# Kernel tuning notes

Hardware: AMD Instinct MI355X
Metric: run time of the kernel (lower is better)

The kernel has to match this reference:

```python
import jax, jax.numpy as jnp
import numpy as np

NUM_HEADS = 4
NUM_GROUPS = 8
EPS = 1e-5


def setup_inputs() -> dict:
    key = jax.random.key(0)
    ks = jax.random.split(key, 4)
    B, C, H, W = 16, 512, 64, 64
    x = jax.random.normal(ks[0], (B, C, H, W), dtype=jnp.float32)
    norm_g = jnp.ones((C,), dtype=jnp.float32)
    norm_b = jnp.zeros((C,), dtype=jnp.float32)
    qkv_w = jax.random.normal(ks[1], (3 * C, C), dtype=jnp.float32) * (1.0 / np.sqrt(C))
    qkv_b = jnp.zeros((3 * C,), dtype=jnp.float32)
    proj_w = jax.random.normal(ks[2], (C, C), dtype=jnp.float32) * (1.0 / np.sqrt(C))
    proj_b = jnp.zeros((C,), dtype=jnp.float32)
    return {"x": x, "norm_g": norm_g, "norm_b": norm_b,
            "qkv_w": qkv_w, "qkv_b": qkv_b, "proj_w": proj_w, "proj_b": proj_b}


def _group_norm(x, g, b):
    B, C, H, W = x.shape
    xg = x.reshape(B, NUM_GROUPS, C // NUM_GROUPS, H, W)
    mean = xg.mean(axis=(2, 3, 4), keepdims=True)
    var = xg.var(axis=(2, 3, 4), keepdims=True)
    xn = ((xg - mean) * jax.lax.rsqrt(var + EPS)).reshape(B, C, H, W)
    return xn * g[None, :, None, None] + b[None, :, None, None]


def reference(x, norm_g, norm_b, qkv_w, qkv_b, proj_w, proj_b):
    B, C, H, W = x.shape
    d = C // NUM_HEADS
    scale = d ** (-0.5)
    xn = _group_norm(x, norm_g, norm_b)
    # 1x1 conv == channel GEMM
    qkv = jnp.einsum('oc,bchw->bohw', qkv_w, xn) + qkv_b[None, :, None, None]
    qkv = qkv.reshape(B, NUM_HEADS, 3 * d, H * W)
    q, k, v = qkv[:, :, :d], qkv[:, :, d:2 * d], qkv[:, :, 2 * d:]
    # Faithful to the original (degenerate) einsum: q's last axis is summed out
    attn = jnp.einsum('bnhq,bnhk->bnhk', q, k) * scale
    attn = jax.nn.softmax(attn, axis=-1)
    out = jnp.einsum('bnhk,bnhv->bnhv', attn, v)
    out = out.reshape(B, C, H, W)
    out = jnp.einsum('oc,bchw->bohw', proj_w, out) + proj_b[None, :, None, None]
    return out + x
```

## Files before the change

kernel.cpp:

```cpp
#include <hip/hip_runtime.h>

#define CC 512
#define SS 4096
#define GELEMS 262144

typedef __attribute__((ext_vector_type(8))) __bf16 bf16x8;
typedef __attribute__((ext_vector_type(4))) float f32x4;
typedef __attribute__((ext_vector_type(4))) unsigned short us4;
typedef __attribute__((ext_vector_type(8))) unsigned short us8;

__device__ __forceinline__ unsigned short f2bf(float f) {
  unsigned int u = __float_as_uint(f);
  u += 0x7fffu + ((u >> 16) & 1u);
  return (unsigned short)(u >> 16);
}
__device__ __forceinline__ int qrow(int cv) { return ((cv >> 7) * 384) + 256 + (cv & 127); }

__device__ __forceinline__ void gl_lds16(const void* g, void* l) {
  __builtin_amdgcn_global_load_lds((const __attribute__((address_space(1))) unsigned int*)g,
                                   (__attribute__((address_space(3))) unsigned int*)l, 16, 0, 0);
}

__global__ __launch_bounds__(256) void k_front(const float* __restrict__ x,
    const float* __restrict__ pw, const float* __restrict__ qw,
    unsigned short* __restrict__ xbft, float* __restrict__ part, float* __restrict__ mw) {
  __shared__ float red[8];
  __shared__ __align__(16) unsigned short G[8 * 512];
  __shared__ __align__(16) unsigned short Asb[64 * 32];
  __shared__ __align__(16) unsigned short Bsb[64 * 32];
  int t = threadIdx.x;
  if (blockIdx.x < 8192) {
    int bid = blockIdx.x;
    int b = bid >> 9, rem = bid & 511, ct = rem >> 6, st = rem & 63;
    int c0 = ct * 64, s0 = st * 64;
    int w = t >> 6, l = t & 63;
    int ch4 = l >> 4, s4 = l & 15;
    int cbase = w * 16 + ch4;
    float4 vv[4];
#pragma unroll
    for (int i = 0; i < 4; ++i) {
      int c = cbase + i * 4;
      vv[i] = *(const float4*)&x[((size_t)(b * 512 + c0 + c)) * SS + s0 + s4 * 4];
    }
    float sm = 0.f, sq = 0.f;
#pragma unroll
    for (int i = 0; i < 4; ++i) {
      sm += vv[i].x + vv[i].y + vv[i].z + vv[i].w;
      sq += vv[i].x * vv[i].x + vv[i].y * vv[i].y + vv[i].z * vv[i].z + vv[i].w * vv[i].w;
    }
#pragma unroll
    for (int off = 32; off; off >>= 1) { sm += __shfl_down(sm, off); sq += __shfl_down(sq, off); }
    if (l == 0) { red[w] = sm; red[4 + w] = sq; }
#pragma unroll
    for (int i = 0; i < 4; ++i) {
      int c = cbase + i * 4, g = c >> 3, chl = c & 7;
      float e[4] = {vv[i].x, vv[i].y, vv[i].z, vv[i].w};
#pragma unroll
      for (int j = 0; j < 4; ++j) {
        int s = s4 * 4 + j, slot = s ^ (s >> 3);
        G[g * 512 + slot * 8 + chl] = f2bf(e[j]);
      }
    }
    __syncthreads();
    if (t == 0) {
      int pidx = (b * 8 + ct) * 64 + st;
      part[pidx * 2] = red[0] + red[1] + red[2] + red[3];
      part[pidx * 2 + 1] = red[4] + red[5] + red[6] + red[7];
    }
    unsigned short* tb = xbft + ((size_t)(b * 64 + st)) * 32768;
    int slot = l ^ (l >> 3);
    int jj = l >> 4, frr = l & 15;
#pragma unroll
    for (int h = 0; h < 2; ++h) {
      int g = w * 2 + h;
      us8 v = *(const us8*)&G[g * 512 + slot * 8];
      int k8g = ct * 8 + g;
      int kc = k8g >> 4, s8l = (k8g >> 2) & 3, fql = k8g & 3;
      *(us8*)&tb[kc * 8192 + (s8l * 4 + jj) * 512 + (fql * 16 + frr) * 8] = v;
    }
  } else {
    int bb = blockIdx.x - 8192;
    int bm = (bb >> 3) * 64;
    int bn = (bb & 7) * 64;
    int w = t >> 6, l = t & 63;
    int wm = (w >> 1) * 32, wn = (w & 1) * 32;
    int fr = l & 15, fk = (l >> 4) * 8;
    f32x4 acc[2][2] = {};
    for (int k0 = 0; k0 < 512; k0 += 32) {
#pragma unroll
      for (int i = 0; i < 2; ++i) {
        int e = i * 256 + t;
        int row = e >> 3, f4 = e & 7;
        float4 v = *(const float4*)&pw[(size_t)(bm + row) * 512 + k0 + f4 * 4];
        us4 pk; pk[0] = f2bf(v.x); pk[1] = f2bf(v.y); pk[2] = f2bf(v.z); pk[3] = f2bf(v.w);
        *(us4*)&Asb[row * 32 + f4 * 4] = pk;
      }
#pragma unroll
      for (int i = 0; i < 2; ++i) {
        int e = i * 256 + t;
        int row = e >> 4, f4 = e & 15;
        float4 v = *(const float4*)&qw[(size_t)qrow(k0 + row) * 512 + bn + f4 * 4];
        Bsb[(f4 * 4 + 0) * 32 + row] = f2bf(v.x);
        Bsb[(f4 * 4 + 1) * 32 + row] = f2bf(v.y);
        Bsb[(f4 * 4 + 2) * 32 + row] = f2bf(v.z);
        Bsb[(f4 * 4 + 3) * 32 + row] = f2bf(v.w);
      }
      __syncthreads();
      bf16x8 a[2], bfr[2];
#pragma unroll
      for (int i = 0; i < 2; ++i) a[i] = *(const bf16x8*)&Asb[(wm + i * 16 + fr) * 32 + fk];
#pragma unroll
      for (int j = 0; j < 2; ++j) bfr[j] = *(const bf16x8*)&Bsb[(wn + j * 16 + fr) * 32 + fk];
#pragma unroll
      for (int i = 0; i < 2; ++i)
#pragma unroll
        for (int j = 0; j < 2; ++j)
          acc[i][j] = __builtin_amdgcn_mfma_f32_16x16x32_bf16(a[i], bfr[j], acc[i][j], 0, 0, 0);
      __syncthreads();
    }
#pragma unroll
    for (int i = 0; i < 2; ++i)
#pragma unroll
      for (int j = 0; j < 2; ++j)
#pragma unroll
        for (int r = 0; r < 4; ++r) {
          int row = bm + wm + i * 16 + (l >> 4) * 4 + r;
          int col = bn + wn + j * 16 + (l & 15);
          mw[(size_t)row * 512 + col] = acc[i][j][r];
        }
  }
}

__global__ __launch_bounds__(256) void k_prep(const float* __restrict__ part,
    const float* __restrict__ ng, const float* __restrict__ nb,
    const float* __restrict__ mw, const float* __restrict__ pw,
    const float* __restrict__ qb, const float* __restrict__ pb,
    unsigned short* __restrict__ mwa, float* __restrict__ bias2) {
  int t = threadIdx.x;
  __shared__ float S1[512], S2[512];
  __shared__ float ms[8], rs[8];
  int b = (blockIdx.x < 2048) ? (blockIdx.x >> 7) : ((blockIdx.x - 2048) >> 3);
  {
    int g = t >> 5, i = t & 31;
    const float* p = part + (size_t)(b * 8 + g) * 128;
    float S = p[i * 2] + p[(i + 32) * 2];
    float Q = p[i * 2 + 1] + p[(i + 32) * 2 + 1];
#pragma unroll
    for (int off = 16; off; off >>= 1) { S += __shfl_down(S, off, 32); Q += __shfl_down(Q, off, 32); }
    if (i == 0) {
      float mean = S * (1.f / 262144.f);
      float var = Q * (1.f / 262144.f) - mean * mean;
      ms[g] = mean; rs[g] = rsqrtf(var + 1e-5f);
    }
  }
  __syncthreads();
  if (blockIdx.x < 2048) {
    int r4 = (blockIdx.x & 127) * 4;
#pragma unroll
    for (int q = 0; q < 2; ++q) { int c = t + q * 256; S1[c] = rs[c >> 6] * ng[c]; }
    __syncthreads();
    int c2 = r4 + (t >> 6), c = (t & 63) * 8;
    const float4* mr = (const float4*)&mw[(size_t)c2 * 512 + c];
    float4 m0 = mr[0], m1 = mr[1];
    const float4* ar = (const float4*)&S1[c];
    float4 a0 = ar[0], a1 = ar[1];
    float v[8] = {m0.x*a0.x, m0.y*a0.y, m0.z*a0.z, m0.w*a0.w,
                  m1.x*a1.x, m1.y*a1.y, m1.z*a1.z, m1.w*a1.w};
    if (c2 >= c && c2 < c + 8) v[c2 - c] += 1.0f;
    us8 o;
#pragma unroll
    for (int j = 0; j < 8; ++j) o[j] = f2bf(v[j]);
    int wblk = c2 >> 6, i2 = (c2 >> 4) & 3, fr = c2 & 15;
    int step = c >> 5, fq = (c >> 3) & 3;
    size_t addr = ((((size_t)(b * 8 + wblk) * 4 + i2) * 16 + step) * 64 + (fq * 16 + fr)) * 8;
    *(us8*)&mwa[addr] = o;
  } else {
    int c2b = ((blockIdx.x - 2048) & 7) * 64;
    int w = t >> 6, l = t & 63;
#pragma unroll
    for (int q = 0; q < 2; ++q) {
      int c = t + q * 256;
      float A = rs[c >> 6] * ng[c];
      S1[c] = nb[c] - ms[c >> 6] * A;
      S2[c] = qb[qrow(c)];
    }
    __syncthreads();
    for (int it = 0; it < 16; ++it) {
      int c2 = c2b + w * 16 + it;
      const float4* pwr = (const float4*)&pw[(size_t)c2 * 512];
      const float4* mwr = (const float4*)&mw[(size_t)c2 * 512];
      float4 p0 = pwr[l * 2], p1 = pwr[l * 2 + 1];
      float4 m0 = mwr[l * 2], m1 = mwr[l * 2 + 1];
      const float4* qs = (const float4*)&S2[l * 8];
      const float4* bs = (const float4*)&S1[l * 8];
      float4 q0 = qs[0], q1 = qs[1], b0 = bs[0], b1 = bs[1];
      float acc = p0.x * q0.x + p0.y * q0.y + p0.z * q0.z + p0.w * q0.w
                + p1.x * q1.x + p1.y * q1.y + p1.z * q1.z + p1.w * q1.w
                + m0.x * b0.x + m0.y * b0.y + m0.z * b0.z + m0.w * b0.w
                + m1.x * b1.x + m1.y * b1.y + m1.z * b1.z + m1.w * b1.w;
#pragma unroll
      for (int off = 32; off; off >>= 1) acc += __shfl_down(acc, off);
      if (l == 0) bias2[b * 512 + c2] = acc + pb[c2];
    }
  }
}

__global__ __launch_bounds__(512, 4) void k_fused5(const unsigned short* __restrict__ mwa,
    const unsigned short* __restrict__ xbft, const float* __restrict__ bias2,
    float* __restrict__ out) {
  __shared__ __align__(16) unsigned short Bs[2][8192];
  int bid0 = blockIdx.x;
  int bid = 1023 - ((bid0 & 7) * 128 + (bid0 >> 3));
  int b = bid >> 6, st = bid & 63;
  int s0 = st * 64;
  int t = threadIdx.x, w = t >> 6, l = t & 63;
  int m0 = w * 64;
  int fr = l & 15, fq = l >> 4;
  const unsigned short* tile = xbft + ((size_t)(b * 64 + st)) * 32768;
  const unsigned short* Ag = mwa + ((size_t)(b * 8 + w)) * 32768;

  auto stage = [&](int buf, int kc) {
    const unsigned short* src = tile + kc * 8192 + w * 1024 + l * 8;
    gl_lds16(src, &Bs[buf][w * 1024]);
    gl_lds16(src + 512, &Bs[buf][w * 1024 + 512]);
  };

  stage(0, 0);
  bf16x8 fa[2][4];
#pragma unroll
  for (int i = 0; i < 4; ++i)
    fa[0][i] = *(const bf16x8*)&Ag[(i * 16 + 0) * 512 + l * 8];
  __syncthreads();

  f32x4 acc[4][4] = {};
#pragma unroll
  for (int kc = 0; kc < 4; ++kc) {
    if (kc < 3) stage((kc + 1) & 1, kc + 1);
#pragma unroll
    for (int s8 = 0; s8 < 4; ++s8) {
      const int step = kc * 4 + s8;
      const int cur = step & 1;
      if (step < 15) {
#pragma unroll
        for (int i = 0; i < 4; ++i)
          fa[cur ^ 1][i] = *(const bf16x8*)&Ag[(i * 16 + step + 1) * 512 + l * 8];
      }
      bf16x8 fb[4];
#pragma unroll
      for (int j = 0; j < 4; ++j)
        fb[j] = *(const bf16x8*)&Bs[kc & 1][(s8 * 4 + j) * 512 + l * 8];
#pragma unroll
      for (int i = 0; i < 4; ++i)
#pragma unroll
        for (int j = 0; j < 4; ++j)
          acc[i][j] = __builtin_amdgcn_mfma_f32_16x16x32_bf16(fa[cur][i], fb[j], acc[i][j], 0, 0, 0);
    }
    if (kc < 3) __syncthreads();
  }

  float4 bi[4];
#pragma unroll
  for (int i = 0; i < 4; ++i)
    bi[i] = *(const float4*)&bias2[b * 512 + m0 + i * 16 + fq * 4];
  __syncthreads();
  float* Ls = (float*)Bs;
  float* ob = out + (size_t)b * 512 * SS + s0;
#pragma unroll
  for (int i = 0; i < 4; ++i) {
    float bir[4] = {bi[i].x, bi[i].y, bi[i].z, bi[i].w};
#pragma unroll
    for (int j = 0; j < 4; ++j)
#pragma unroll
      for (int r = 0; r < 4; ++r)
        Ls[w * 1024 + (fq * 4 + r) * 64 + (((j ^ fq) & 3) * 16 + fr)] = acc[i][j][r] + bir[r];
    asm volatile("s_waitcnt lgkmcnt(0)" ::: "memory");
    __builtin_amdgcn_sched_barrier(0);
#pragma unroll
    for (int q = 0; q < 4; ++q) {
      int row16 = q * 4 + (l >> 4);
      int colR = (l & 15) * 4;
      f32x4 v = *(const f32x4*)&Ls[w * 1024 + row16 * 64 + (colR ^ (q * 16))];
      __builtin_nontemporal_store(v, (f32x4*)&ob[(size_t)(m0 + i * 16 + row16) * SS + colR]);
    }
    asm volatile("s_waitcnt lgkmcnt(0)" ::: "memory");
  }
}

__global__ __launch_bounds__(256) void k_stats(const float* __restrict__ x, float* __restrict__ part) {
  int bid = blockIdx.x;
  int bg = bid >> 3, sp = bid & 7;
  const float4* p = (const float4*)(x + (size_t)bg * GELEMS + (size_t)sp * 32768);
  int t = threadIdx.x;
  float s = 0.f, ss = 0.f;
#pragma unroll
  for (int i = 0; i < 32; ++i) {
    float4 v = p[i * 256 + t];
    s += v.x + v.y + v.z + v.w;
    ss += v.x * v.x + v.y * v.y + v.z * v.z + v.w * v.w;
  }
#pragma unroll
  for (int off = 32; off; off >>= 1) { s += __shfl_down(s, off); ss += __shfl_down(ss, off); }
  __shared__ float red[8];
  int wid = t >> 6;
  if ((t & 63) == 0) { red[wid * 2] = s; red[wid * 2 + 1] = ss; }
  __syncthreads();
  if (t == 0) {
    part[bid * 2] = red[0] + red[2] + red[4] + red[6];
    part[bid * 2 + 1] = red[1] + red[3] + red[5] + red[7];
  }
}

__global__ __launch_bounds__(256) void k_mw(const float* __restrict__ pw, const float* __restrict__ qw,
                                            float* __restrict__ mw, unsigned short* __restrict__ mwbf) {
  __shared__ __align__(16) unsigned short Asb[64 * 32];
  __shared__ __align__(16) unsigned short Bsb[64 * 32];
  int t = threadIdx.x;
  int bm = (blockIdx.x >> 3) * 64;
  int bn = (blockIdx.x & 7) * 64;
  int w = t >> 6, l = t & 63;
  int wm = (w >> 1) * 32, wn = (w & 1) * 32;
  int fr = l & 15, fk = (l >> 4) * 8;
  f32x4 acc[2][2] = {};
  for (int k0 = 0; k0 < 512; k0 += 32) {
#pragma unroll
    for (int i = 0; i < 2; ++i) {
      int e = i * 256 + t;
      int row = e >> 3, f4 = e & 7;
      float4 v = *(const float4*)&pw[(size_t)(bm + row) * 512 + k0 + f4 * 4];
      us4 pk; pk[0] = f2bf(v.x); pk[1] = f2bf(v.y); pk[2] = f2bf(v.z); pk[3] = f2bf(v.w);
      *(us4*)&Asb[row * 32 + f4 * 4] = pk;
    }
#pragma unroll
    for (int i = 0; i < 2; ++i) {
      int e = i * 256 + t;
      int row = e >> 4, f4 = e & 15;
      float4 v = *(const float4*)&qw[(size_t)qrow(k0 + row) * 512 + bn + f4 * 4];
      Bsb[(f4 * 4 + 0) * 32 + row] = f2bf(v.x);
      Bsb[(f4 * 4 + 1) * 32 + row] = f2bf(v.y);
      Bsb[(f4 * 4 + 2) * 32 + row] = f2bf(v.z);
      Bsb[(f4 * 4 + 3) * 32 + row] = f2bf(v.w);
    }
    __syncthreads();
    bf16x8 a[2], bfr[2];
#pragma unroll
    for (int i = 0; i < 2; ++i) a[i] = *(const bf16x8*)&Asb[(wm + i * 16 + fr) * 32 + fk];
#pragma unroll
    for (int j = 0; j < 2; ++j) bfr[j] = *(const bf16x8*)&Bsb[(wn + j * 16 + fr) * 32 + fk];
#pragma unroll
    for (int i = 0; i < 2; ++i)
#pragma unroll
      for (int j = 0; j < 2; ++j)
        acc[i][j] = __builtin_amdgcn_mfma_f32_16x16x32_bf16(a[i], bfr[j], acc[i][j], 0, 0, 0);
    __syncthreads();
  }
#pragma unroll
  for (int i = 0; i < 2; ++i)
#pragma unroll
    for (int j = 0; j < 2; ++j)
#pragma unroll
      for (int r = 0; r < 4; ++r) {
        int row = bm + wm + i * 16 + (l >> 4) * 4 + r;
        int col = bn + wn + j * 16 + (l & 15);
        float v = acc[i][j][r];
        mw[(size_t)row * 512 + col] = v;
        mwbf[(size_t)row * 512 + col] = f2bf(v);
      }
}

__global__ __launch_bounds__(256) void k_fin(const float* __restrict__ part,
    const float* __restrict__ ng, const float* __restrict__ nb,
    float* __restrict__ afac, float* __restrict__ bcv, int np) {
  int b = blockIdx.x, t = threadIdx.x;
  __shared__ float mean_s[8], rstd_s[8];
  int g = t >> 5, i = t & 31;
  float S = 0.f, Q = 0.f;
  for (int k = i; k < np; k += 32) {
    S += part[((b * 8 + g) * np + k) * 2];
    Q += part[((b * 8 + g) * np + k) * 2 + 1];
  }
#pragma unroll
  for (int off = 16; off; off >>= 1) { S += __shfl_down(S, off, 32); Q += __shfl_down(Q, off, 32); }
  if (i == 0) {
    float mean = S * (1.f / 262144.f);
    float var = Q * (1.f / 262144.f) - mean * mean;
    mean_s[g] = mean;
    rstd_s[g] = rsqrtf(var + 1e-5f);
  }
  __syncthreads();
#pragma unroll
  for (int q = 0; q < 2; ++q) {
    int c = t + q * 256;
    int gg = c >> 6;
    float A = rstd_s[gg] * ng[c];
    afac[b * 512 + c] = A;
    bcv[b * 512 + c] = nb[c] - mean_s[gg] * A;
  }
}

__global__ __launch_bounds__(256) void k_bias2(const float* __restrict__ mw,
    const float* __restrict__ bcv, const float* __restrict__ pw,
    const float* __restrict__ qb, const float* __restrict__ pb, float* __restrict__ bias2) {
  int b = blockIdx.x >> 3, c2b = (blockIdx.x & 7) * 64;
  int t = threadIdx.x, w = t >> 6, l = t & 63;
  __shared__ float Bcs[512], Qbs[512];
  for (int i = t; i < 512; i += 256) { Bcs[i] = bcv[b * 512 + i]; Qbs[i] = qb[qrow(i)]; }
  __syncthreads();
  for (int it = 0; it < 16; ++it) {
    int c2 = c2b + w * 16 + it;
    const float4* pwr = (const float4*)&pw[(size_t)c2 * 512];
    const float4* mwr = (const float4*)&mw[(size_t)c2 * 512];
    float4 p0 = pwr[l * 2], p1 = pwr[l * 2 + 1];
    float4 m0 = mwr[l * 2], m1 = mwr[l * 2 + 1];
    const float4* qs = (const float4*)&Qbs[l * 8];
    const float4* bs = (const float4*)&Bcs[l * 8];
    float4 q0 = qs[0], q1 = qs[1], b0 = bs[0], b1 = bs[1];
    float acc = p0.x * q0.x + p0.y * q0.y + p0.z * q0.z + p0.w * q0.w
              + p1.x * q1.x + p1.y * q1.y + p1.z * q1.z + p1.w * q1.w
              + m0.x * b0.x + m0.y * b0.y + m0.z * b0.z + m0.w * b0.w
              + m1.x * b1.x + m1.y * b1.y + m1.z * b1.z + m1.w * b1.w;
#pragma unroll
    for (int off = 32; off; off >>= 1) acc += __shfl_down(acc, off);
    if (l == 0) bias2[b * 512 + c2] = acc + pb[c2];
  }
}

__global__ __launch_bounds__(256) void k_gemm_fb(const unsigned short* __restrict__ mwbf,
    const float* __restrict__ x, const float* __restrict__ afac,
    const float* __restrict__ bias2, float* __restrict__ out) {
  __shared__ __align__(16) unsigned short Ab[128 * 32];
  __shared__ __align__(16) unsigned short Bb[128 * 32];
  __shared__ float Afs[512];
  int bid0 = blockIdx.x;
  int bid = (bid0 & 7) * 256 + (bid0 >> 3);
  int b = bid >> 7, rem = bid & 127, nt = rem >> 2, mt = rem & 3;
  int m0 = mt * 128, s0 = nt * 128;
  int t = threadIdx.x, w = t >> 6, l = t & 63;
  int wm = (w >> 1) * 64, wn = (w & 1) * 64;
  const unsigned short* Ag = mwbf + (size_t)m0 * CC;
  int lr = l >> 2, lk = (l & 3) * 8;
  int fr = l & 15, fk = (l >> 4) * 8;
  for (int i = t; i < 512; i += 256) Afs[i] = afac[b * CC + i];
  __syncthreads();
  f32x4 acc[4][4] = {};
  for (int k0 = 0; k0 < CC; k0 += 32) {
#pragma unroll
    for (int q = 0; q < 2; ++q) {
      int row = w * 32 + q * 16;
      gl_lds16(Ag + (size_t)(row + lr) * CC + k0 + lk, &Ab[row * 32]);
    }
#pragma unroll
    for (int i2 = 0; i2 < 4; ++i2) {
      int e = i2 * 256 + t;
      int row = e >> 5, f4 = e & 31;
      float4 v = *(const float4*)&x[((size_t)(b * CC + k0 + row)) * SS + s0 + f4 * 4];
      float a = Afs[k0 + row];
      Bb[(f4 * 4 + 0) * 32 + row] = f2bf(v.x * a);
      Bb[(f4 * 4 + 1) * 32 + row] = f2bf(v.y * a);
      Bb[(f4 * 4 + 2) * 32 + row] = f2bf(v.z * a);
      Bb[(f4 * 4 + 3) * 32 + row] = f2bf(v.w * a);
    }
    __syncthreads();
    bf16x8 af[4], bfr[4];
#pragma unroll
    for (int i = 0; i < 4; ++i) af[i] = *(const bf16x8*)&Ab[(wm + i * 16 + fr) * 32 + fk];
#pragma unroll
    for (int j = 0; j < 4; ++j) bfr[j] = *(const bf16x8*)&Bb[(wn + j * 16 + fr) * 32 + fk];
#pragma unroll
    for (int i = 0; i < 4; ++i)
#pragma unroll
      for (int j = 0; j < 4; ++j)
        acc[i][j] = __builtin_amdgcn_mfma_f32_16x16x32_bf16(af[i], bfr[j], acc[i][j], 0, 0, 0);
    __syncthreads();
  }
  int c2b = m0 + wm, sb = s0 + wn;
  float bi[4][4];
#pragma unroll
  for (int i = 0; i < 4; ++i)
#pragma unroll
    for (int r = 0; r < 4; ++r)
      bi[i][r] = bias2[b * CC + c2b + i * 16 + (l >> 4) * 4 + r];
#pragma unroll
  for (int i = 0; i < 4; ++i)
#pragma unroll
    for (int j = 0; j < 4; ++j)
#pragma unroll
      for (int r = 0; r < 4; ++r) {
        int c2 = c2b + i * 16 + (l >> 4) * 4 + r;
        int s = sb + j * 16 + (l & 15);
        size_t oi = ((size_t)(b * CC + c2)) * SS + s;
        out[oi] = acc[i][j][r] + bi[i][r] + x[oi];
      }
}

extern "C" void kernel_launch(void* const* d_in, const int* in_sizes, int n_in,
                              void* d_out, int out_size, void* d_ws, size_t ws_size,
                              hipStream_t stream) {
  const float* x = (const float*)d_in[0];
  const float* ng = (const float*)d_in[1];
  const float* nb = (const float*)d_in[2];
  const float* qw = (const float*)d_in[3];
  const float* qb = (const float*)d_in[4];
  const float* pw = (const float*)d_in[5];
  const float* pb = (const float*)d_in[6];
  float* out = (float*)d_out;
  char* ws = (char*)d_ws;

  float* part = (float*)(ws + 0);
  float* afac = (float*)(ws + 65536);
  float* bcv = (float*)(ws + 98304);
  float* bias2 = (float*)(ws + 131072);
  float* mw = (float*)(ws + 163840);
  unsigned short* mwbf = (unsigned short*)(ws + 1212416);
  unsigned short* mwa = (unsigned short*)(ws + 1736704);
  unsigned short* xbft = (unsigned short*)(ws + 10125312);

  bool fast = ws_size >= 77234176ull;

  if (fast) {
    k_front<<<8256, 256, 0, stream>>>(x, pw, qw, xbft, part, mw);
    k_prep<<<2176, 256, 0, stream>>>(part, ng, nb, mw, pw, qb, pb, mwa, bias2);
    k_fused5<<<1024, 512, 0, stream>>>(mwa, xbft, bias2, out);
  } else {
    k_stats<<<1024, 256, 0, stream>>>(x, part);
    k_mw<<<64, 256, 0, stream>>>(pw, qw, mw, mwbf);
    k_fin<<<16, 256, 0, stream>>>(part, ng, nb, afac, bcv, 8);
    k_bias2<<<128, 256, 0, stream>>>(mw, bcv, pw, qb, pb, bias2);
    k_gemm_fb<<<2048, 256, 0, stream>>>(mwbf, x, afac, bias2, out);
  }
}
```

Measured before the change: 121.3 us.

## Coarsen front transpose blocks to process 16 channels over 1024 positions

The x-to-bf16 transpose and statistics part of k_front now has each block handle 16 channels across 1024 spatial positions, looping over four chunks. The block count drops from 8192 to 2048, and each block emits one partial-stats pair instead of one per 64x64 tile. k_prep is adjusted to reduce 16 partials per group instead of 64. The aim is to cut per-block launch overhead and partial-stats traffic. In exchange there are more barriers per block and less parallelism for hiding memory latency.

Result: slower. 128.9 us (+6.3%).

```diff
diff --git a/kernel.cpp b/kernel.cpp
--- a/kernel.cpp
+++ b/kernel.cpp
@@ -25,64 +25,69 @@
     const float* __restrict__ pw, const float* __restrict__ qw,
     unsigned short* __restrict__ xbft, float* __restrict__ part, float* __restrict__ mw) {
   __shared__ float red[8];
-  __shared__ __align__(16) unsigned short G[8 * 512];
+  __shared__ __align__(16) unsigned short G[2 * 256 * 8];
   __shared__ __align__(16) unsigned short Asb[64 * 32];
   __shared__ __align__(16) unsigned short Bsb[64 * 32];
   int t = threadIdx.x;
-  if (blockIdx.x < 8192) {
+  int w = t >> 6, l = t & 63;
+  if (blockIdx.x < 2048) {
     int bid = blockIdx.x;
-    int b = bid >> 9, rem = bid & 511, ct = rem >> 6, st = rem & 63;
-    int c0 = ct * 64, s0 = st * 64;
-    int w = t >> 6, l = t & 63;
-    int ch4 = l >> 4, s4 = l & 15;
-    int cbase = w * 16 + ch4;
-    float4 vv[4];
-#pragma unroll
-    for (int i = 0; i < 4; ++i) {
-      int c = cbase + i * 4;
-      vv[i] = *(const float4*)&x[((size_t)(b * 512 + c0 + c)) * SS + s0 + s4 * 4];
-    }
-    float sm = 0.f, sq = 0.f;
-#pragma unroll
-    for (int i = 0; i < 4; ++i) {
-      sm += vv[i].x + vv[i].y + vv[i].z + vv[i].w;
-      sq += vv[i].x * vv[i].x + vv[i].y * vv[i].y + vv[i].z * vv[i].z + vv[i].w * vv[i].w;
-    }
-#pragma unroll
-    for (int off = 32; off; off >>= 1) { sm += __shfl_down(sm, off); sq += __shfl_down(sq, off); }
-    if (l == 0) { red[w] = sm; red[4 + w] = sq; }
-#pragma unroll
-    for (int i = 0; i < 4; ++i) {
-      int c = cbase + i * 4, g = c >> 3, chl = c & 7;
-      float e[4] = {vv[i].x, vv[i].y, vv[i].z, vv[i].w};
-#pragma unroll
-      for (int j = 0; j < 4; ++j) {
-        int s = s4 * 4 + j, slot = s ^ (s >> 3);
-        G[g * 512 + slot * 8 + chl] = f2bf(e[j]);
-      }
-    }
+    int b = bid >> 7, rem = bid & 127, c16 = rem >> 2, sq = rem & 3;
+    int c0 = c16 * 16;
+    int t4 = t >> 4, sl = t & 15;
+    int gl = t4 >> 3, chl = t4 & 7;
+    const float* xb = x + ((size_t)(b * 512 + c0 + t4)) * SS + (size_t)sq * 1024;
+    float sm = 0.f, sqa = 0.f;
+#pragma unroll 1
+    for (int chunk = 0; chunk < 4; ++chunk) {
+      float4 v[4];
+#pragma unroll
+      for (int i = 0; i < 4; ++i)
+        v[i] = *(const float4*)&xb[chunk * 256 + i * 64 + sl * 4];
+#pragma unroll
+      for (int i = 0; i < 4; ++i) {
+        sm += v[i].x + v[i].y + v[i].z + v[i].w;
+        sqa += v[i].x * v[i].x + v[i].y * v[i].y + v[i].z * v[i].z + v[i].w * v[i].w;
+      }
+#pragma unroll
+      for (int i = 0; i < 4; ++i) {
+        float e[4] = {v[i].x, v[i].y, v[i].z, v[i].w};
+#pragma unroll
+        for (int j = 0; j < 4; ++j) {
+          int s6 = sl * 4 + j;
+          int slot = i * 64 + (s6 ^ (s6 >> 3));
+          G[(gl * 256 + slot) * 8 + chl] = f2bf(e[j]);
+        }
+      }
+      __syncthreads();
+      {
+        int slot = w * 64 + (l ^ (l >> 3));
+        int st = sq * 16 + chunk * 4 + w;
+        unsigned short* tb = xbft + ((size_t)(b * 64 + st)) * 32768;
+        int jj = l >> 4, frr = l & 15;
+#pragma unroll
+        for (int h = 0; h < 2; ++h) {
+          us8 v8 = *(const us8*)&G[(h * 256 + slot) * 8];
+          int g = c16 * 2 + h;
+          int kc = g >> 4, s8l = (g >> 2) & 3, fql = g & 3;
+          *(us8*)&tb[kc * 8192 + (s8l * 4 + jj) * 512 + (fql * 16 + frr) * 8] = v8;
+        }
+      }
+      __syncthreads();
+    }
+#pragma unroll
+    for (int off = 32; off; off >>= 1) { sm += __shfl_down(sm, off); sqa += __shfl_down(sqa, off); }
+    if (l == 0) { red[w] = sm; red[4 + w] = sqa; }
     __syncthreads();
     if (t == 0) {
-      int pidx = (b * 8 + ct) * 64 + st;
+      int pidx = (b * 32 + c16) * 4 + sq;
       part[pidx * 2] = red[0] + red[1] + red[2] + red[3];
       part[pidx * 2 + 1] = red[4] + red[5] + red[6] + red[7];
     }
-    unsigned short* tb = xbft + ((size_t)(b * 64 + st)) * 32768;
-    int slot = l ^ (l >> 3);
-    int jj = l >> 4, frr = l & 15;
-#pragma unroll
-    for (int h = 0; h < 2; ++h) {
-      int g = w * 2 + h;
-      us8 v = *(const us8*)&G[g * 512 + slot * 8];
-      int k8g = ct * 8 + g;
-      int kc = k8g >> 4, s8l = (k8g >> 2) & 3, fql = k8g & 3;
-      *(us8*)&tb[kc * 8192 + (s8l * 4 + jj) * 512 + (fql * 16 + frr) * 8] = v;
-    }
   } else {
-    int bb = blockIdx.x - 8192;
+    int bb = blockIdx.x - 2048;
     int bm = (bb >> 3) * 64;
     int bn = (bb & 7) * 64;
-    int w = t >> 6, l = t & 63;
     int wm = (w >> 1) * 32, wn = (w & 1) * 32;
     int fr = l & 15, fk = (l >> 4) * 8;
     f32x4 acc[2][2] = {};
@@ -142,9 +147,9 @@
   int b = (blockIdx.x < 2048) ? (blockIdx.x >> 7) : ((blockIdx.x - 2048) >> 3);
   {
     int g = t >> 5, i = t & 31;
-    const float* p = part + (size_t)(b * 8 + g) * 128;
-    float S = p[i * 2] + p[(i + 32) * 2];
-    float Q = p[i * 2 + 1] + p[(i + 32) * 2 + 1];
+    const float* p = part + (size_t)(b * 8 + g) * 32;
+    float S = 0.f, Q = 0.f;
+    if (i < 16) { S = p[i * 2]; Q = p[i * 2 + 1]; }
 #pragma unroll
     for (int off = 16; off; off >>= 1) { S += __shfl_down(S, off, 32); Q += __shfl_down(Q, off, 32); }
     if (i == 0) {
@@ -517,7 +522,7 @@
   bool fast = ws_size >= 77234176ull;
 
   if (fast) {
-    k_front<<<8256, 256, 0, stream>>>(x, pw, qw, xbft, part, mw);
+    k_front<<<2112, 256, 0, stream>>>(x, pw, qw, xbft, part, mw);
     k_prep<<<2176, 256, 0, stream>>>(part, ng, nb, mw, pw, qb, pb, mwa, bias2);
     k_fused5<<<1024, 512, 0, stream>>>(mwa, xbft, bias2, out);
   } else {
```

## Restructure front stats/transpose kernel into fewer blocks looping over 8-channel groups

Applied to the files above, without the earlier changes.

The stats-and-bf16-transpose part of k_front moves from 8192 small blocks (64 channels by 64 spatial each) to 1024 blocks. Each block covers one 8-channel slice of a batch over the full spatial range and loops over 8 chunks with LDS staging. Partial sums become one per 8-channel slice, and k_prep reads 8 partials per group instead of 64. This cuts block launch overhead and partial-sum traffic, but adds two barriers per chunk and serialises the loads inside each block.

Result: no change. 123.6 us (+1.9%).

```diff
diff --git a/kernel.cpp b/kernel.cpp
--- a/kernel.cpp
+++ b/kernel.cpp
@@ -25,64 +25,72 @@
     const float* __restrict__ pw, const float* __restrict__ qw,
     unsigned short* __restrict__ xbft, float* __restrict__ part, float* __restrict__ mw) {
   __shared__ float red[8];
-  __shared__ __align__(16) unsigned short G[8 * 512];
+  __shared__ __align__(16) unsigned short G[512 * 8];
   __shared__ __align__(16) unsigned short Asb[64 * 32];
   __shared__ __align__(16) unsigned short Bsb[64 * 32];
   int t = threadIdx.x;
-  if (blockIdx.x < 8192) {
+  int w = t >> 6, l = t & 63;
+  if (blockIdx.x < 1024) {
     int bid = blockIdx.x;
-    int b = bid >> 9, rem = bid & 511, ct = rem >> 6, st = rem & 63;
-    int c0 = ct * 64, s0 = st * 64;
-    int w = t >> 6, l = t & 63;
-    int ch4 = l >> 4, s4 = l & 15;
-    int cbase = w * 16 + ch4;
-    float4 vv[4];
-#pragma unroll
-    for (int i = 0; i < 4; ++i) {
-      int c = cbase + i * 4;
-      vv[i] = *(const float4*)&x[((size_t)(b * 512 + c0 + c)) * SS + s0 + s4 * 4];
-    }
+    int b = bid >> 6, g8 = bid & 63;
+    int c0 = g8 * 8, chl0 = 2 * w;
+    const float* r0 = x + ((size_t)(b * 512 + c0 + chl0)) * SS;
+    const float* r1 = r0 + SS;
+    int kc = g8 >> 4, s8l = (g8 >> 2) & 3, fql = g8 & 3;
+    int toff = kc * 8192 + s8l * 4 * 512 + fql * 128;
     float sm = 0.f, sq = 0.f;
-#pragma unroll
-    for (int i = 0; i < 4; ++i) {
-      sm += vv[i].x + vv[i].y + vv[i].z + vv[i].w;
-      sq += vv[i].x * vv[i].x + vv[i].y * vv[i].y + vv[i].z * vv[i].z + vv[i].w * vv[i].w;
+#pragma unroll 1
+    for (int chunk = 0; chunk < 8; ++chunk) {
+      float4 v0[2], v1[2];
+#pragma unroll
+      for (int i = 0; i < 2; ++i) v0[i] = *(const float4*)&r0[chunk * 512 + (i * 64 + l) * 4];
+#pragma unroll
+      for (int i = 0; i < 2; ++i) v1[i] = *(const float4*)&r1[chunk * 512 + (i * 64 + l) * 4];
+#pragma unroll
+      for (int i = 0; i < 2; ++i) {
+        sm += v0[i].x + v0[i].y + v0[i].z + v0[i].w + v1[i].x + v1[i].y + v1[i].z + v1[i].w;
+        sq += v0[i].x * v0[i].x + v0[i].y * v0[i].y + v0[i].z * v0[i].z + v0[i].w * v0[i].w
+            + v1[i].x * v1[i].x + v1[i].y * v1[i].y + v1[i].z * v1[i].z + v1[i].w * v1[i].w;
+      }
+#pragma unroll
+      for (int i = 0; i < 2; ++i) {
+        float e0[4] = {v0[i].x, v0[i].y, v0[i].z, v0[i].w};
+        float e1[4] = {v1[i].x, v1[i].y, v1[i].z, v1[i].w};
+#pragma unroll
+        for (int j = 0; j < 4; ++j) {
+          int sl_ = i * 256 + l * 4 + j;
+          int sub = sl_ >> 6, s6 = sl_ & 63;
+          int slot = s6 ^ (s6 >> 3);
+          G[(sub * 64 + slot) * 8 + chl0] = f2bf(e0[j]);
+          G[(sub * 64 + slot) * 8 + chl0 + 1] = f2bf(e1[j]);
+        }
+      }
+      __syncthreads();
+#pragma unroll
+      for (int h = 0; h < 2; ++h) {
+        int sl_ = t + h * 256;
+        int sub = sl_ >> 6, s6 = sl_ & 63;
+        int slot = s6 ^ (s6 >> 3);
+        us8 v8 = *(const us8*)&G[(sub * 64 + slot) * 8];
+        int st = chunk * 8 + sub;
+        unsigned short* tb = xbft + ((size_t)(b * 64 + st)) * 32768;
+        int jj = s6 >> 4, frr = s6 & 15;
+        *(us8*)&tb[toff + jj * 512 + frr * 8] = v8;
+      }
+      __syncthreads();
     }
 #pragma unroll
     for (int off = 32; off; off >>= 1) { sm += __shfl_down(sm, off); sq += __shfl_down(sq, off); }
     if (l == 0) { red[w] = sm; red[4 + w] = sq; }
-#pragma unroll
-    for (int i = 0; i < 4; ++i) {
-      int c = cbase + i * 4, g = c >> 3, chl = c & 7;
-      float e[4] = {vv[i].x, vv[i].y, vv[i].z, vv[i].w};
-#pragma unroll
-      for (int j = 0; j < 4; ++j) {
-        int s = s4 * 4 + j, slot = s ^ (s >> 3);
-        G[g * 512 + slot * 8 + chl] = f2bf(e[j]);
-      }
-    }
     __syncthreads();
     if (t == 0) {
-      int pidx = (b * 8 + ct) * 64 + st;
-      part[pidx * 2] = red[0] + red[1] + red[2] + red[3];
-      part[pidx * 2 + 1] = red[4] + red[5] + red[6] + red[7];
-    }
-    unsigned short* tb = xbft + ((size_t)(b * 64 + st)) * 32768;
-    int slot = l ^ (l >> 3);
-    int jj = l >> 4, frr = l & 15;
-#pragma unroll
-    for (int h = 0; h < 2; ++h) {
-      int g = w * 2 + h;
-      us8 v = *(const us8*)&G[g * 512 + slot * 8];
-      int k8g = ct * 8 + g;
-      int kc = k8g >> 4, s8l = (k8g >> 2) & 3, fql = k8g & 3;
-      *(us8*)&tb[kc * 8192 + (s8l * 4 + jj) * 512 + (fql * 16 + frr) * 8] = v;
+      part[(b * 64 + g8) * 2] = red[0] + red[1] + red[2] + red[3];
+      part[(b * 64 + g8) * 2 + 1] = red[4] + red[5] + red[6] + red[7];
     }
   } else {
-    int bb = blockIdx.x - 8192;
+    int bb = blockIdx.x - 1024;
     int bm = (bb >> 3) * 64;
     int bn = (bb & 7) * 64;
-    int w = t >> 6, l = t & 63;
     int wm = (w >> 1) * 32, wn = (w & 1) * 32;
     int fr = l & 15, fk = (l >> 4) * 8;
     f32x4 acc[2][2] = {};
@@ -142,9 +150,9 @@
   int b = (blockIdx.x < 2048) ? (blockIdx.x >> 7) : ((blockIdx.x - 2048) >> 3);
   {
     int g = t >> 5, i = t & 31;
-    const float* p = part + (size_t)(b * 8 + g) * 128;
-    float S = p[i * 2] + p[(i + 32) * 2];
-    float Q = p[i * 2 + 1] + p[(i + 32) * 2 + 1];
+    const float* p = part + ((size_t)(b * 64 + g * 8)) * 2;
+    float S = 0.f, Q = 0.f;
+    if (i < 8) { S = p[i * 2]; Q = p[i * 2 + 1]; }
 #pragma unroll
     for (int off = 16; off; off >>= 1) { S += __shfl_down(S, off, 32); Q += __shfl_down(Q, off, 32); }
     if (i == 0) {
@@ -517,7 +525,7 @@
   bool fast = ws_size >= 77234176ull;
 
   if (fast) {
-    k_front<<<8256, 256, 0, stream>>>(x, pw, qw, xbft, part, mw);
+    k_front<<<1088, 256, 0, stream>>>(x, pw, qw, xbft, part, mw);
     k_prep<<<2176, 256, 0, stream>>>(part, ng, nb, mw, pw, qb, pb, mwa, bias2);
     k_fused5<<<1024, 512, 0, stream>>>(mwa, xbft, bias2, out);
   } else {
```
